# Kernel optimization log

Measured on AMD Instinct MI355X. Metric: run time of the kernel, lower is better.

Reference implementation:

```python
import jax, jax.numpy as jnp
import numpy as np

REG_COEF = 25.0


def _reflect(points, planes):
    # points: [B,P,3], planes: [B,4] -> reflected points [B,P,3]
    normals = planes[:, 0:3] / jnp.linalg.norm(planes[:, 0:3], axis=1, keepdims=True)
    offsets = planes[:, 3]
    # signed distance of each point to the plane: [B,P]
    dist = jnp.einsum('bd,bpd->bp', normals, points) + offsets[:, None]
    return points - 2.0 * dist[..., None] * normals[:, None, :]


def _chamfer(x, y):
    # x,y: [B,P,3]; pytorch3d chamfer_distance default:
    # mean over points, mean over batch, sum of both directions (squared dists)
    x2 = jnp.sum(x * x, axis=-1)  # [B,P]
    y2 = jnp.sum(y * y, axis=-1)  # [B,P]
    # pairwise squared distances [B,P,P]
    d = x2[:, :, None] + y2[:, None, :] - 2.0 * jnp.einsum('bpd,bqd->bpq', x, y)
    d = jnp.maximum(d, 0.0)
    cham_x = jnp.mean(jnp.min(d, axis=2))  # x -> nearest in y
    cham_y = jnp.mean(jnp.min(d, axis=1))  # y -> nearest in x
    return cham_x + cham_y


def _reg_loss(planes):
    # planes: [B,H,4]
    normals = planes[:, :, :3]
    normals = normals / jnp.linalg.norm(normals, axis=2, keepdims=True)
    H = normals.shape[1]
    a = jnp.einsum('bhd,bgd->bhg', normals, normals) - jnp.eye(H, dtype=normals.dtype)
    # Frobenius norm per batch -> [B]
    return jnp.sqrt(jnp.sum(a * a, axis=(1, 2)))


def setup_inputs() -> dict:
    key = jax.random.key(0)
    k1, k2 = jax.random.split(key)
    B, H, P = 8, 3, 4096
    return {
        'predicted_planes': jax.random.normal(k1, (B, H, 4), dtype=jnp.float32),
        'sample_points': jax.random.normal(k2, (B, P, 3), dtype=jnp.float32),
        'voxel_grids': jnp.zeros((B, 32, 32, 32), dtype=jnp.float32),
        'cp_grids': jnp.zeros((B, 32, 32, 32), dtype=jnp.float32),
    }


def reference(predicted_planes, sample_points, voxel_grids, cp_grids):
    n_heads = predicted_planes.shape[1]
    reg = jnp.sum(_reg_loss(predicted_planes))
    refl = jnp.asarray(0.0, dtype=sample_points.dtype)
    for h in range(n_heads):  # small fixed head count (3)
        reflected = _reflect(sample_points, predicted_planes[:, h, :])
        refl = refl + _chamfer(sample_points, reflected)
    return refl + REG_COEF * reg
```

## Files before the change

kernel.cpp:

```cpp
#include <hip/hip_runtime.h>
#include <math.h>

#define NB 8
#define NH 3
#define NBH 24
#define NP 4096
#define BLK 256
#define RPB 128
#define ROWBLKS (NP / RPB)

typedef _Float16 half8 __attribute__((ext_vector_type(8)));
typedef float floatx16 __attribute__((ext_vector_type(16)));

#define MIN3(r, a, b) asm("v_min3_f32 %0, %0, %1, %2" : "+v"(r) : "v"(a), "v"(b))

#define MFMA16(d, a, bb, c) \
    asm("v_mfma_f32_32x32x16_f16 %0, %1, %2, %3" : "=&v"(d) : "v"(a), "v"(bb), "v"(c))

__global__ void reg_kernel(const float* __restrict__ planes, float* __restrict__ out) {
    const int l = threadIdx.x;
    float r = 0.0f;
    if (l < NB) {
        float n[NH][3];
        for (int hh = 0; hh < NH; ++hh) {
            const float* pl = planes + (l * NH + hh) * 4;
            float a0 = pl[0], a1 = pl[1], a2 = pl[2];
            float inv = 1.0f / sqrtf(a0 * a0 + a1 * a1 + a2 * a2);
            n[hh][0] = a0 * inv; n[hh][1] = a1 * inv; n[hh][2] = a2 * inv;
        }
        float fro = 0.0f;
        for (int i = 0; i < NH; ++i)
            for (int j = 0; j < NH; ++j) {
                float d = n[i][0] * n[j][0] + n[i][1] * n[j][1] + n[i][2] * n[j][2]
                          - (i == j ? 1.0f : 0.0f);
                fro += d * d;
            }
        r = 25.0f * sqrtf(fro);
    }
    for (int o = 32; o; o >>= 1) r += __shfl_down(r, o);
    if (l == 0) out[0] = r;
}

__global__ void __launch_bounds__(BLK, 3) chamfer_mfma(const float* __restrict__ pts,
                                                       const float* __restrict__ planes,
                                                       float* __restrict__ out) {
    __shared__ _Float16 qcols[NP * 4];
    __shared__ float rsqbuf[RPB];
    __shared__ float bsum[4];

    const int tid  = threadIdx.x;
    const int lane = tid & 63;
    const int wave = tid >> 6;
    const int bh   = blockIdx.y;
    const int b    = bh / NH;

    const float* pl = planes + bh * 4;
    float n0 = pl[0], n1 = pl[1], n2 = pl[2], off = pl[3];
    float inv = 1.0f / sqrtf(n0 * n0 + n1 * n1 + n2 * n2);
    n0 *= inv; n1 *= inv; n2 *= inv;

    const float* bp = pts + (size_t)b * NP * 3;
    const int h = lane >> 5;

    for (int i = tid; i < NP; i += BLK) {
        float y0 = bp[i * 3 + 0], y1 = bp[i * 3 + 1], y2 = bp[i * 3 + 2];
        float t = 2.0f * (n0 * y0 + n1 * y1 + n2 * y2 + off);
        y0 -= t * n0; y1 -= t * n1; y2 -= t * n2;
        float csq = y0 * y0 + y1 * y1 + y2 * y2;
        _Float16* q = &qcols[i * 4];
        q[0] = (_Float16)(-2.0f * y0); q[1] = (_Float16)(-2.0f * y1);
        q[2] = (_Float16)(-2.0f * y2); q[3] = (_Float16)csq;
    }

    const int rlocal = wave * 32 + (lane & 31);
    const int row = blockIdx.x * RPB + rlocal;
    half8 Aev = {0, 0, 0, 0, 0, 0, 0, 0};
    half8 Aod = {0, 0, 0, 0, 0, 0, 0, 0};
    {
        float a0 = bp[row * 3 + 0], a1 = bp[row * 3 + 1], a2 = bp[row * 3 + 2];
        if (lane < 32) {
            rsqbuf[rlocal] = a0 * a0 + a1 * a1 + a2 * a2;
            Aev[0] = (_Float16)a0; Aev[1] = (_Float16)a1;
            Aev[2] = (_Float16)a2; Aev[3] = (_Float16)1.0f;
            Aod[4] = (_Float16)a0; Aod[5] = (_Float16)a1;
            Aod[6] = (_Float16)a2; Aod[7] = (_Float16)1.0f;
        }
    }
    __syncthreads();

    floatx16 crsq;
    #pragma unroll
    for (int j = 0; j < 16; ++j)
        crsq[j] = rsqbuf[wave * 32 + (j & 3) + 8 * (j >> 2) + 4 * h];

    float rm[16];
    #pragma unroll
    for (int j = 0; j < 16; ++j) rm[j] = 1e30f;

    const _Float16* bcol = &qcols[(lane & 31) * 8];
    #define LD(u) (*(const half8*)(bcol + (u) * 256))

    half8 c0 = LD(0), c1 = LD(1), c2 = LD(2), c3 = LD(3);
    floatx16 dA0, dA1, dB0, dB1;
    MFMA16(dA0, Aev, c0, crsq);  MFMA16(dA1, Aod, c0, crsq);
    MFMA16(dB0, Aev, c1, crsq);  MFMA16(dB1, Aod, c1, crsq);

    #pragma unroll 1
    for (int u = 4; u <= 60; u += 4) {
        c0 = LD(u);
        #pragma unroll
        for (int j = 0; j < 16; ++j) MIN3(rm[j], dA0[j], dA1[j]);
        MFMA16(dA0, Aev, c2, crsq);  MFMA16(dA1, Aod, c2, crsq);
        c1 = LD(u + 1);
        #pragma unroll
        for (int j = 0; j < 16; ++j) MIN3(rm[j], dB0[j], dB1[j]);
        MFMA16(dB0, Aev, c3, crsq);  MFMA16(dB1, Aod, c3, crsq);
        c2 = LD(u + 2);
        #pragma unroll
        for (int j = 0; j < 16; ++j) MIN3(rm[j], dA0[j], dA1[j]);
        MFMA16(dA0, Aev, c0, crsq);  MFMA16(dA1, Aod, c0, crsq);
        c3 = LD(u + 3);
        #pragma unroll
        for (int j = 0; j < 16; ++j) MIN3(rm[j], dB0[j], dB1[j]);
        MFMA16(dB0, Aev, c1, crsq);  MFMA16(dB1, Aod, c1, crsq);
    }
    {
        #pragma unroll
        for (int j = 0; j < 16; ++j) MIN3(rm[j], dA0[j], dA1[j]);
        MFMA16(dA0, Aev, c2, crsq);  MFMA16(dA1, Aod, c2, crsq);
        #pragma unroll
        for (int j = 0; j < 16; ++j) MIN3(rm[j], dB0[j], dB1[j]);
        MFMA16(dB0, Aev, c3, crsq);  MFMA16(dB1, Aod, c3, crsq);
        #pragma unroll
        for (int j = 0; j < 16; ++j) MIN3(rm[j], dA0[j], dA1[j]);
        #pragma unroll
        for (int j = 0; j < 16; ++j) MIN3(rm[j], dB0[j], dB1[j]);
    }
    #undef LD

    #pragma unroll
    for (int j = 0; j < 16; ++j) {
        float v = rm[j];
        v = fminf(v, __shfl_xor(v, 1));
        v = fminf(v, __shfl_xor(v, 2));
        v = fminf(v, __shfl_xor(v, 4));
        v = fminf(v, __shfl_xor(v, 8));
        v = fminf(v, __shfl_xor(v, 16));
        rm[j] = v;
    }
    float s = 0.0f;
    #pragma unroll
    for (int j = 0; j < 16; ++j) s += fmaxf(rm[j], 0.0f);
    s += __shfl_xor(s, 32);

    if (lane == 0) bsum[wave] = s;
    __syncthreads();
    if (tid == 0)
        atomicAdd(out, (bsum[0] + bsum[1] + bsum[2] + bsum[3]) * (2.0f / (float)(NB * NP)));
}

extern "C" void kernel_launch(void* const* d_in, const int* in_sizes, int n_in,
                              void* d_out, int out_size, void* d_ws, size_t ws_size,
                              hipStream_t stream) {
    const float* planes = (const float*)d_in[0];
    const float* pts    = (const float*)d_in[1];
    float* out          = (float*)d_out;

    reg_kernel<<<1, 64, 0, stream>>>(planes, out);

    dim3 grid(ROWBLKS, NBH);
    chamfer_mfma<<<grid, BLK, 0, stream>>>(pts, planes, out);
}
```

Baseline: 79.81 us.

## Precompute reflected fp16 columns in prep kernel, split columns across waves, drop LDS

A new prep kernel computes the reflected, fp16-packed column data once per (batch, head) into global workspace and also absorbs the regularization loss. The chamfer kernel stops rebuilding this 32KB LDS table in every block and instead loads the columns from global/L2. Each block now covers 64 rows, with the two column halves split across waves and combined through a small LDS min. This removes redundant per-block reflection work and the LDS pressure that limited occupancy, at the cost of global-memory reads in the MFMA inner loop and an extra workspace round trip.

```diff
diff --git a/kernel.cpp b/kernel.cpp
--- a/kernel.cpp
+++ b/kernel.cpp
@@ -6,53 +6,27 @@
 #define NBH 24
 #define NP 4096
 #define BLK 256
-#define RPB 128
+#define RPB 64
 #define ROWBLKS (NP / RPB)
 
+typedef _Float16 half4 __attribute__((ext_vector_type(4)));
 typedef _Float16 half8 __attribute__((ext_vector_type(8)));
 typedef float floatx16 __attribute__((ext_vector_type(16)));
 
+#define MIN3(r, a, b) asm("v_min3_f32 %0, %0, %1, %2" : "+v"(r) : "v"(a), "v"(bb_##a), "v"(b))
+#undef MIN3
 #define MIN3(r, a, b) asm("v_min3_f32 %0, %0, %1, %2" : "+v"(r) : "v"(a), "v"(b))
 
 #define MFMA16(d, a, bb, c) \
     asm("v_mfma_f32_32x32x16_f16 %0, %1, %2, %3" : "=&v"(d) : "v"(a), "v"(bb), "v"(c))
 
-__global__ void reg_kernel(const float* __restrict__ planes, float* __restrict__ out) {
-    const int l = threadIdx.x;
-    float r = 0.0f;
-    if (l < NB) {
-        float n[NH][3];
-        for (int hh = 0; hh < NH; ++hh) {
-            const float* pl = planes + (l * NH + hh) * 4;
-            float a0 = pl[0], a1 = pl[1], a2 = pl[2];
-            float inv = 1.0f / sqrtf(a0 * a0 + a1 * a1 + a2 * a2);
-            n[hh][0] = a0 * inv; n[hh][1] = a1 * inv; n[hh][2] = a2 * inv;
-        }
-        float fro = 0.0f;
-        for (int i = 0; i < NH; ++i)
-            for (int j = 0; j < NH; ++j) {
-                float d = n[i][0] * n[j][0] + n[i][1] * n[j][1] + n[i][2] * n[j][2]
-                          - (i == j ? 1.0f : 0.0f);
-                fro += d * d;
-            }
-        r = 25.0f * sqrtf(fro);
-    }
-    for (int o = 32; o; o >>= 1) r += __shfl_down(r, o);
-    if (l == 0) out[0] = r;
-}
-
-__global__ void __launch_bounds__(BLK, 3) chamfer_mfma(const float* __restrict__ pts,
-                                                       const float* __restrict__ planes,
-                                                       float* __restrict__ out) {
-    __shared__ _Float16 qcols[NP * 4];
-    __shared__ float rsqbuf[RPB];
-    __shared__ float bsum[4];
-
-    const int tid  = threadIdx.x;
-    const int lane = tid & 63;
-    const int wave = tid >> 6;
-    const int bh   = blockIdx.y;
-    const int b    = bh / NH;
+__global__ void __launch_bounds__(256) prep_kernel(const float* __restrict__ pts,
+                                                   const float* __restrict__ planes,
+                                                   _Float16* __restrict__ qg,
+                                                   float* __restrict__ out) {
+    const int tid = threadIdx.x;
+    const int bh  = blockIdx.x >> 2;
+    const int b   = bh / NH;
 
     const float* pl = planes + bh * 4;
     float n0 = pl[0], n1 = pl[1], n2 = pl[2], off = pl[3];
@@ -60,53 +34,93 @@
     n0 *= inv; n1 *= inv; n2 *= inv;
 
     const float* bp = pts + (size_t)b * NP * 3;
-    const int h = lane >> 5;
-
-    for (int i = tid; i < NP; i += BLK) {
+    const int base = (blockIdx.x & 3) * 1024 + tid;
+    #pragma unroll
+    for (int k = 0; k < 4; ++k) {
+        const int i = base + k * 256;
         float y0 = bp[i * 3 + 0], y1 = bp[i * 3 + 1], y2 = bp[i * 3 + 2];
         float t = 2.0f * (n0 * y0 + n1 * y1 + n2 * y2 + off);
         y0 -= t * n0; y1 -= t * n1; y2 -= t * n2;
         float csq = y0 * y0 + y1 * y1 + y2 * y2;
-        _Float16* q = &qcols[i * 4];
-        q[0] = (_Float16)(-2.0f * y0); q[1] = (_Float16)(-2.0f * y1);
-        q[2] = (_Float16)(-2.0f * y2); q[3] = (_Float16)csq;
+        half4 q = { (_Float16)(-2.0f * y0), (_Float16)(-2.0f * y1),
+                    (_Float16)(-2.0f * y2), (_Float16)csq };
+        *(half4*)(qg + ((size_t)bh * NP + i) * 4) = q;
     }
 
-    const int rlocal = wave * 32 + (lane & 31);
+    if (blockIdx.x == 0 && tid >= 192) {
+        const int l = tid - 192;
+        float r = 0.0f;
+        if (l < NB) {
+            float n[NH][3];
+            for (int hh = 0; hh < NH; ++hh) {
+                const float* p2 = planes + (l * NH + hh) * 4;
+                float a0 = p2[0], a1 = p2[1], a2 = p2[2];
+                float iv = 1.0f / sqrtf(a0 * a0 + a1 * a1 + a2 * a2);
+                n[hh][0] = a0 * iv; n[hh][1] = a1 * iv; n[hh][2] = a2 * iv;
+            }
+            float fro = 0.0f;
+            for (int i = 0; i < NH; ++i)
+                for (int j = 0; j < NH; ++j) {
+                    float d = n[i][0] * n[j][0] + n[i][1] * n[j][1] + n[i][2] * n[j][2]
+                              - (i == j ? 1.0f : 0.0f);
+                    fro += d * d;
+                }
+            r = 25.0f * sqrtf(fro);
+        }
+        for (int o = 32; o; o >>= 1) r += __shfl_down(r, o);
+        if (l == 0) out[0] = r;
+    }
+}
+
+__global__ void __launch_bounds__(BLK, 6) chamfer_mfma(const float* __restrict__ pts,
+                                                       const _Float16* __restrict__ qg,
+                                                       float* __restrict__ out) {
+    __shared__ float rowmin[2][RPB];
+
+    const int tid  = threadIdx.x;
+    const int lane = tid & 63;
+    const int wave = tid >> 6;
+    const int bh   = blockIdx.y;
+    const int b    = bh / NH;
+    const int rw   = wave & 1;
+    const int cw   = wave >> 1;
+    const int h    = lane >> 5;
+
+    const float* bp = pts + (size_t)b * NP * 3;
+
+    const int rlocal = rw * 32 + (lane & 31);
     const int row = blockIdx.x * RPB + rlocal;
+    float a0 = bp[row * 3 + 0], a1 = bp[row * 3 + 1], a2 = bp[row * 3 + 2];
+    float rsq = a0 * a0 + a1 * a1 + a2 * a2;
     half8 Aev = {0, 0, 0, 0, 0, 0, 0, 0};
     half8 Aod = {0, 0, 0, 0, 0, 0, 0, 0};
-    {
-        float a0 = bp[row * 3 + 0], a1 = bp[row * 3 + 1], a2 = bp[row * 3 + 2];
-        if (lane < 32) {
-            rsqbuf[rlocal] = a0 * a0 + a1 * a1 + a2 * a2;
-            Aev[0] = (_Float16)a0; Aev[1] = (_Float16)a1;
-            Aev[2] = (_Float16)a2; Aev[3] = (_Float16)1.0f;
-            Aod[4] = (_Float16)a0; Aod[5] = (_Float16)a1;
-            Aod[6] = (_Float16)a2; Aod[7] = (_Float16)1.0f;
-        }
+    if (lane < 32) {
+        Aev[0] = (_Float16)a0; Aev[1] = (_Float16)a1;
+        Aev[2] = (_Float16)a2; Aev[3] = (_Float16)1.0f;
+        Aod[4] = (_Float16)a0; Aod[5] = (_Float16)a1;
+        Aod[6] = (_Float16)a2; Aod[7] = (_Float16)1.0f;
     }
-    __syncthreads();
 
     floatx16 crsq;
     #pragma unroll
     for (int j = 0; j < 16; ++j)
-        crsq[j] = rsqbuf[wave * 32 + (j & 3) + 8 * (j >> 2) + 4 * h];
+        crsq[j] = __shfl(rsq, (j & 3) + 8 * (j >> 2) + 4 * h);
 
     float rm[16];
     #pragma unroll
     for (int j = 0; j < 16; ++j) rm[j] = 1e30f;
 
-    const _Float16* bcol = &qcols[(lane & 31) * 8];
-    #define LD(u) (*(const half8*)(bcol + (u) * 256))
+    const _Float16* bcol = qg + (size_t)bh * NP * 4 + (lane & 31) * 8;
+    const int U0 = cw * 32;
+    #define LD(u) (*(const half8*)(bcol + (size_t)(u) * 256))
 
-    half8 c0 = LD(0), c1 = LD(1), c2 = LD(2), c3 = LD(3);
+    half8 c0 = LD(U0), c1 = LD(U0 + 1), c2 = LD(U0 + 2), c3 = LD(U0 + 3);
     floatx16 dA0, dA1, dB0, dB1;
     MFMA16(dA0, Aev, c0, crsq);  MFMA16(dA1, Aod, c0, crsq);
     MFMA16(dB0, Aev, c1, crsq);  MFMA16(dB1, Aod, c1, crsq);
 
     #pragma unroll 1
-    for (int u = 4; u <= 60; u += 4) {
+    for (int u = U0 + 4; u <= U0 + 28; u += 4) {
         c0 = LD(u);
         #pragma unroll
         for (int j = 0; j < 16; ++j) MIN3(rm[j], dA0[j], dA1[j]);
@@ -148,15 +162,20 @@
         v = fminf(v, __shfl_xor(v, 16));
         rm[j] = v;
     }
-    float s = 0.0f;
-    #pragma unroll
-    for (int j = 0; j < 16; ++j) s += fmaxf(rm[j], 0.0f);
-    s += __shfl_xor(s, 32);
 
-    if (lane == 0) bsum[wave] = s;
+    if ((lane & 31) == 0) {
+        #pragma unroll
+        for (int j = 0; j < 16; ++j)
+            rowmin[cw][rw * 32 + (j & 3) + 8 * (j >> 2) + 4 * h] = rm[j];
+    }
     __syncthreads();
-    if (tid == 0)
-        atomicAdd(out, (bsum[0] + bsum[1] + bsum[2] + bsum[3]) * (2.0f / (float)(NB * NP)));
+
+    if (tid < RPB) {
+        float v = fmaxf(fminf(rowmin[0][tid], rowmin[1][tid]), 0.0f);
+        #pragma unroll
+        for (int o = 32; o; o >>= 1) v += __shfl_down(v, o);
+        if (tid == 0) atomicAdd(out, v * (2.0f / (float)(NB * NP)));
+    }
 }
 
 extern "C" void kernel_launch(void* const* d_in, const int* in_sizes, int n_in,
@@ -165,9 +184,10 @@
     const float* planes = (const float*)d_in[0];
     const float* pts    = (const float*)d_in[1];
     float* out          = (float*)d_out;
+    _Float16* qg        = (_Float16*)d_ws;
 
-    reg_kernel<<<1, 64, 0, stream>>>(planes, out);
+    prep_kernel<<<96, 256, 0, stream>>>(pts, planes, qg, out);
 
     dim3 grid(ROWBLKS, NBH);
-    chamfer_mfma<<<grid, BLK, 0, stream>>>(pts, planes, out);
+    chamfer_mfma<<<grid, BLK, 0, stream>>>(pts, qg, out);
 }
```

After: 266.8 us. 234% more time.

## Hoist row-norm term out of MFMA accumulator and replace atomics with finalize kernel

Applied to the files above, without the earlier changes.

Since the row's squared norm is constant along each min-reduction row, it is dropped from the MFMA C operand (now zero) and added after the min via a lane shuffle. This frees the 16-register crsq accumulator input and the LDS staging buffer, allowing launch bounds to rise from 3 to 4 blocks per SIMD. The float atomicAdd into the output is replaced by per-block partials in workspace plus a single finalize kernel that also computes the regulariser, replacing the separate reg kernel. The clamp to zero now happens after the min rather than per element, which is equivalent since max(x,0) is monotonic.

```diff
diff --git a/kernel.cpp b/kernel.cpp
--- a/kernel.cpp
+++ b/kernel.cpp
@@ -8,44 +8,20 @@
 #define BLK 256
 #define RPB 128
 #define ROWBLKS (NP / RPB)
+#define NPART (ROWBLKS * NBH)
 
 typedef _Float16 half8 __attribute__((ext_vector_type(8)));
 typedef float floatx16 __attribute__((ext_vector_type(16)));
 
 #define MIN3(r, a, b) asm("v_min3_f32 %0, %0, %1, %2" : "+v"(r) : "v"(a), "v"(b))
 
-#define MFMA16(d, a, bb, c) \
-    asm("v_mfma_f32_32x32x16_f16 %0, %1, %2, %3" : "=&v"(d) : "v"(a), "v"(bb), "v"(c))
+#define MFMA16Z(d, a, bb) \
+    asm("v_mfma_f32_32x32x16_f16 %0, %1, %2, 0" : "=&v"(d) : "v"(a), "v"(bb))
 
-__global__ void reg_kernel(const float* __restrict__ planes, float* __restrict__ out) {
-    const int l = threadIdx.x;
-    float r = 0.0f;
-    if (l < NB) {
-        float n[NH][3];
-        for (int hh = 0; hh < NH; ++hh) {
-            const float* pl = planes + (l * NH + hh) * 4;
-            float a0 = pl[0], a1 = pl[1], a2 = pl[2];
-            float inv = 1.0f / sqrtf(a0 * a0 + a1 * a1 + a2 * a2);
-            n[hh][0] = a0 * inv; n[hh][1] = a1 * inv; n[hh][2] = a2 * inv;
-        }
-        float fro = 0.0f;
-        for (int i = 0; i < NH; ++i)
-            for (int j = 0; j < NH; ++j) {
-                float d = n[i][0] * n[j][0] + n[i][1] * n[j][1] + n[i][2] * n[j][2]
-                          - (i == j ? 1.0f : 0.0f);
-                fro += d * d;
-            }
-        r = 25.0f * sqrtf(fro);
-    }
-    for (int o = 32; o; o >>= 1) r += __shfl_down(r, o);
-    if (l == 0) out[0] = r;
-}
-
-__global__ void __launch_bounds__(BLK, 3) chamfer_mfma(const float* __restrict__ pts,
+__global__ void __launch_bounds__(BLK, 4) chamfer_mfma(const float* __restrict__ pts,
                                                        const float* __restrict__ planes,
-                                                       float* __restrict__ out) {
+                                                       float* __restrict__ partials) {
     __shared__ _Float16 qcols[NP * 4];
-    __shared__ float rsqbuf[RPB];
     __shared__ float bsum[4];
 
     const int tid  = threadIdx.x;
@@ -53,6 +29,7 @@
     const int wave = tid >> 6;
     const int bh   = blockIdx.y;
     const int b    = bh / NH;
+    const int h    = lane >> 5;
 
     const float* pl = planes + bh * 4;
     float n0 = pl[0], n1 = pl[1], n2 = pl[2], off = pl[3];
@@ -60,7 +37,6 @@
     n0 *= inv; n1 *= inv; n2 *= inv;
 
     const float* bp = pts + (size_t)b * NP * 3;
-    const int h = lane >> 5;
 
     for (int i = tid; i < NP; i += BLK) {
         float y0 = bp[i * 3 + 0], y1 = bp[i * 3 + 1], y2 = bp[i * 3 + 2];
@@ -72,26 +48,18 @@
         q[2] = (_Float16)(-2.0f * y2); q[3] = (_Float16)csq;
     }
 
-    const int rlocal = wave * 32 + (lane & 31);
-    const int row = blockIdx.x * RPB + rlocal;
+    const int row = blockIdx.x * RPB + wave * 32 + (lane & 31);
+    float a0 = bp[row * 3 + 0], a1 = bp[row * 3 + 1], a2 = bp[row * 3 + 2];
+    float rsqv = a0 * a0 + a1 * a1 + a2 * a2;
     half8 Aev = {0, 0, 0, 0, 0, 0, 0, 0};
     half8 Aod = {0, 0, 0, 0, 0, 0, 0, 0};
-    {
-        float a0 = bp[row * 3 + 0], a1 = bp[row * 3 + 1], a2 = bp[row * 3 + 2];
-        if (lane < 32) {
-            rsqbuf[rlocal] = a0 * a0 + a1 * a1 + a2 * a2;
-            Aev[0] = (_Float16)a0; Aev[1] = (_Float16)a1;
-            Aev[2] = (_Float16)a2; Aev[3] = (_Float16)1.0f;
-            Aod[4] = (_Float16)a0; Aod[5] = (_Float16)a1;
-            Aod[6] = (_Float16)a2; Aod[7] = (_Float16)1.0f;
-        }
+    if (lane < 32) {
+        Aev[0] = (_Float16)a0; Aev[1] = (_Float16)a1;
+        Aev[2] = (_Float16)a2; Aev[3] = (_Float16)1.0f;
+        Aod[4] = (_Float16)a0; Aod[5] = (_Float16)a1;
+        Aod[6] = (_Float16)a2; Aod[7] = (_Float16)1.0f;
     }
     __syncthreads();
-
-    floatx16 crsq;
-    #pragma unroll
-    for (int j = 0; j < 16; ++j)
-        crsq[j] = rsqbuf[wave * 32 + (j & 3) + 8 * (j >> 2) + 4 * h];
 
     float rm[16];
     #pragma unroll
@@ -102,35 +70,35 @@
 
     half8 c0 = LD(0), c1 = LD(1), c2 = LD(2), c3 = LD(3);
     floatx16 dA0, dA1, dB0, dB1;
-    MFMA16(dA0, Aev, c0, crsq);  MFMA16(dA1, Aod, c0, crsq);
-    MFMA16(dB0, Aev, c1, crsq);  MFMA16(dB1, Aod, c1, crsq);
+    MFMA16Z(dA0, Aev, c0);  MFMA16Z(dA1, Aod, c0);
+    MFMA16Z(dB0, Aev, c1);  MFMA16Z(dB1, Aod, c1);
 
     #pragma unroll 1
     for (int u = 4; u <= 60; u += 4) {
         c0 = LD(u);
         #pragma unroll
         for (int j = 0; j < 16; ++j) MIN3(rm[j], dA0[j], dA1[j]);
-        MFMA16(dA0, Aev, c2, crsq);  MFMA16(dA1, Aod, c2, crsq);
+        MFMA16Z(dA0, Aev, c2);  MFMA16Z(dA1, Aod, c2);
         c1 = LD(u + 1);
         #pragma unroll
         for (int j = 0; j < 16; ++j) MIN3(rm[j], dB0[j], dB1[j]);
-        MFMA16(dB0, Aev, c3, crsq);  MFMA16(dB1, Aod, c3, crsq);
+        MFMA16Z(dB0, Aev, c3);  MFMA16Z(dB1, Aod, c3);
         c2 = LD(u + 2);
         #pragma unroll
         for (int j = 0; j < 16; ++j) MIN3(rm[j], dA0[j], dA1[j]);
-        MFMA16(dA0, Aev, c0, crsq);  MFMA16(dA1, Aod, c0, crsq);
+        MFMA16Z(dA0, Aev, c0);  MFMA16Z(dA1, Aod, c0);
         c3 = LD(u + 3);
         #pragma unroll
         for (int j = 0; j < 16; ++j) MIN3(rm[j], dB0[j], dB1[j]);
-        MFMA16(dB0, Aev, c1, crsq);  MFMA16(dB1, Aod, c1, crsq);
+        MFMA16Z(dB0, Aev, c1);  MFMA16Z(dB1, Aod, c1);
     }
     {
         #pragma unroll
         for (int j = 0; j < 16; ++j) MIN3(rm[j], dA0[j], dA1[j]);
-        MFMA16(dA0, Aev, c2, crsq);  MFMA16(dA1, Aod, c2, crsq);
+        MFMA16Z(dA0, Aev, c2);  MFMA16Z(dA1, Aod, c2);
         #pragma unroll
         for (int j = 0; j < 16; ++j) MIN3(rm[j], dB0[j], dB1[j]);
-        MFMA16(dB0, Aev, c3, crsq);  MFMA16(dB1, Aod, c3, crsq);
+        MFMA16Z(dB0, Aev, c3);  MFMA16Z(dB1, Aod, c3);
         #pragma unroll
         for (int j = 0; j < 16; ++j) MIN3(rm[j], dA0[j], dA1[j]);
         #pragma unroll
@@ -148,15 +116,54 @@
         v = fminf(v, __shfl_xor(v, 16));
         rm[j] = v;
     }
+
     float s = 0.0f;
     #pragma unroll
-    for (int j = 0; j < 16; ++j) s += fmaxf(rm[j], 0.0f);
+    for (int j = 0; j < 16; ++j) {
+        float rsqj = __shfl(rsqv, (j & 3) + 8 * (j >> 2) + 4 * h);
+        s += fmaxf(rm[j] + rsqj, 0.0f);
+    }
     s += __shfl_xor(s, 32);
 
     if (lane == 0) bsum[wave] = s;
     __syncthreads();
     if (tid == 0)
-        atomicAdd(out, (bsum[0] + bsum[1] + bsum[2] + bsum[3]) * (2.0f / (float)(NB * NP)));
+        partials[blockIdx.y * ROWBLKS + blockIdx.x] =
+            bsum[0] + bsum[1] + bsum[2] + bsum[3];
+}
+
+__global__ void __launch_bounds__(256) finalize(const float* __restrict__ planes,
+                                                const float* __restrict__ partials,
+                                                float* __restrict__ out) {
+    __shared__ float acc[4];
+    const int tid = threadIdx.x;
+    float s = partials[tid] + partials[tid + 256] + partials[tid + 512];
+    #pragma unroll
+    for (int o = 32; o; o >>= 1) s += __shfl_down(s, o);
+    if ((tid & 63) == 0) acc[tid >> 6] = s;
+    __syncthreads();
+    if (tid == 0) {
+        float cham = (acc[0] + acc[1] + acc[2] + acc[3]) * (2.0f / (float)(NB * NP));
+        float reg = 0.0f;
+        for (int bb = 0; bb < NB; ++bb) {
+            float n[NH][3];
+            for (int hh = 0; hh < NH; ++hh) {
+                const float* p2 = planes + (bb * NH + hh) * 4;
+                float a0 = p2[0], a1 = p2[1], a2 = p2[2];
+                float iv = 1.0f / sqrtf(a0 * a0 + a1 * a1 + a2 * a2);
+                n[hh][0] = a0 * iv; n[hh][1] = a1 * iv; n[hh][2] = a2 * iv;
+            }
+            float fro = 0.0f;
+            for (int i = 0; i < NH; ++i)
+                for (int j = 0; j < NH; ++j) {
+                    float d = n[i][0] * n[j][0] + n[i][1] * n[j][1] + n[i][2] * n[j][2]
+                              - (i == j ? 1.0f : 0.0f);
+                    fro += d * d;
+                }
+            reg += 25.0f * sqrtf(fro);
+        }
+        out[0] = cham + reg;
+    }
 }
 
 extern "C" void kernel_launch(void* const* d_in, const int* in_sizes, int n_in,
@@ -165,9 +172,9 @@
     const float* planes = (const float*)d_in[0];
     const float* pts    = (const float*)d_in[1];
     float* out          = (float*)d_out;
-
-    reg_kernel<<<1, 64, 0, stream>>>(planes, out);
+    float* partials     = (float*)d_ws;
 
     dim3 grid(ROWBLKS, NBH);
-    chamfer_mfma<<<grid, BLK, 0, stream>>>(pts, planes, out);
+    chamfer_mfma<<<grid, BLK, 0, stream>>>(pts, planes, partials);
+    finalize<<<1, 256, 0, stream>>>(planes, partials, out);
 }
```

Result: no change. 79.05 us (-1.0%).
